# Kernel optimization log

Hardware: AMD Instinct MI355X
Metric: run time of the kernel (lower is better)

Reference implementation:

```python
import jax, jax.numpy as jnp
import numpy as np

EPS = 1e-6
MIN_EIG = 1e-4
TAU = 1.0  # obs_temperature


def _expm(A):
    """Batched matrix exponential for small KxK matrices via scaling-and-squaring
    + 12-term Taylor (matches torch.linalg.matrix_exp to ~1e-6 for moderate norms).
    Fully differentiable in both modes. A: (..., K, K)."""
    s = 6
    A = A * (1.0 / 2.0 ** s)
    I = jnp.eye(A.shape[-1], dtype=A.dtype)
    E = I + A
    term = A
    for k in range(2, 13):
        term = jnp.matmul(term, A) / k
        E = E + term
    for _ in range(s):
        E = jnp.matmul(E, E)
    return E


def setup_inputs() -> dict:
    key = jax.random.key(0)
    ks = jax.random.split(key, 6)
    B, N, K, V = 1, 2048, 3, 8192
    I = jnp.eye(K, dtype=jnp.float32)
    Ap = jax.random.normal(ks[0], (B, N, K, K), jnp.float32)
    Sigma_prior = Ap @ jnp.swapaxes(Ap, -1, -2) / K + 0.5 * I  # SPD
    Aq = jax.random.normal(ks[1], (B, N, K, K), jnp.float32)
    Sigma_q = Aq @ jnp.swapaxes(Aq, -1, -2) / K + 0.5 * I  # SPD
    phi = 0.5 * jax.random.normal(ks[2], (B, N, 3), jnp.float32)
    beta = jax.nn.softmax(jax.random.normal(ks[3], (B, N, N), jnp.float32), axis=-1)
    mu = jax.random.normal(ks[4], (B, N, K), jnp.float32)
    W_out = jax.random.normal(ks[5], (V, K), jnp.float32) / jnp.sqrt(float(K))
    generators = jnp.array([[[0, 0, 0], [0, 0, -1], [0, 1, 0]],
                            [[0, 0, 1], [0, 0, 0], [-1, 0, 0]],
                            [[0, -1, 0], [1, 0, 0], [0, 0, 0]]], jnp.float32)
    return dict(Sigma_prior=Sigma_prior, Sigma_q=Sigma_q, phi=phi, beta=beta,
                mu=mu, W_out=W_out, generators=generators)


def reference(Sigma_prior, Sigma_q, phi, beta, mu, W_out, generators):
    B, N, K = mu.shape
    dt = Sigma_prior.dtype
    I = jnp.eye(K, dtype=dt)

    # Prior precision Lambda_p = (Sigma_p + eps I)^{-1}
    Lambda_p = jnp.linalg.inv(Sigma_prior + EPS * I)

    # Categorical observation precision: Lambda_o = Cov_p(W) / tau^2
    logits = jnp.einsum('bnk,vk->bnv', mu, W_out) / TAU
    p = jax.nn.softmax(logits, axis=-1)                                # (B,N,V)
    mean_w = jnp.einsum('bnv,vk->bnk', p, W_out)                        # E_p[w]
    second = jnp.einsum('bnv,vk,vl->bnkl', p, W_out, W_out)             # E_p[ww^T]
    Lambda_o = (second - jnp.einsum('bnk,bnl->bnkl', mean_w, mean_w)) / TAU ** 2
    Lambda_o = 0.5 * (Lambda_o + jnp.swapaxes(Lambda_o, -1, -2)) + EPS * I

    # Posterior precision
    Lambda_q = jnp.linalg.inv(Sigma_q + EPS * I)                        # (B,N,K,K)

    # Gauge transport Omega_{ij} = e^{phi_i} e^{-phi_j}
    phi_mat = jnp.einsum('bnc,ckl->bnkl', phi, generators)              # (B,N,K,K)
    exp_phi = _expm(phi_mat)
    exp_neg_phi = _expm(-phi_mat)
    Omega = jnp.einsum('bikl,bjlm->bijkm', exp_phi, exp_neg_phi)        # (B,N,N,K,K)

    # Transported precision Lambda~_{qj in i-frame} = Omega Lambda_q Omega^T
    Lt = jnp.einsum('bijkl,bjlm,bijnm->bijkn', Omega, Lambda_q, Omega)  # (B,N,N,K,K)
    M_incoming = jnp.einsum('bij,bijkn->bikn', beta, Lt)                # (B,N,K,K)

    # Outgoing recoil: (sum_j beta_{ji}) * Lambda_{qi}
    M_outgoing = beta.sum(axis=1)[..., None, None] * Lambda_q

    M = Lambda_p + Lambda_o + M_incoming + M_outgoing
    M = 0.5 * (M + jnp.swapaxes(M, -1, -2))
    bad = ~jnp.isfinite(M)
    M = jnp.where(bad, jnp.broadcast_to(I, M.shape), M)
    M = M + max(MIN_EIG, 1e-4) * I

    # Eigenvalue floor and inverse
    w, v = jnp.linalg.eigh(M.astype(jnp.float32))
    w = jnp.clip(w, MIN_EIG, None)
    M_pd = jnp.einsum('...ij,...j,...kj->...ik', v, w, v)
    M_inv = jnp.einsum('...ij,...j,...kj->...ik', v, 1.0 / w, v)
    return M_pd.astype(dt), M_inv.astype(dt)
```

## Files before the change

kernel.cpp:

```cpp
#include <hip/hip_runtime.h>
#include <math.h>

#define EPSV 1e-6f
#define MINEIG 1e-4f


__device__ __forceinline__ void mm3(const float a[3][3], const float b[3][3], float c[3][3]) {
#pragma unroll
  for (int i = 0; i < 3; ++i)
#pragma unroll
    for (int j = 0; j < 3; ++j)
      c[i][j] = fmaf(a[i][0], b[0][j], fmaf(a[i][1], b[1][j], a[i][2] * b[2][j]));
}

__device__ __forceinline__ void inv3(const float a[3][3], float inv[3][3]) {
  float c00 = a[1][1] * a[2][2] - a[1][2] * a[2][1];
  float c01 = -(a[1][0] * a[2][2] - a[1][2] * a[2][0]);
  float c02 = a[1][0] * a[2][1] - a[1][1] * a[2][0];
  float det = a[0][0] * c00 + a[0][1] * c01 + a[0][2] * c02;
  float id = 1.0f / det;
  inv[0][0] = c00 * id;
  inv[0][1] = (a[0][2] * a[2][1] - a[0][1] * a[2][2]) * id;
  inv[0][2] = (a[0][1] * a[1][2] - a[0][2] * a[1][1]) * id;
  inv[1][0] = c01 * id;
  inv[1][1] = (a[0][0] * a[2][2] - a[0][2] * a[2][0]) * id;
  inv[1][2] = (a[0][2] * a[1][0] - a[0][0] * a[1][2]) * id;
  inv[2][0] = c02 * id;
  inv[2][1] = (a[0][1] * a[2][0] - a[0][0] * a[2][1]) * id;
  inv[2][2] = (a[0][0] * a[1][1] - a[0][1] * a[1][0]) * id;
}

__device__ void expm3(const float A[3][3], float E[3][3]) {
  float As[3][3], term[3][3], tmp[3][3];
#pragma unroll
  for (int i = 0; i < 3; ++i)
#pragma unroll
    for (int j = 0; j < 3; ++j) {
      As[i][j] = A[i][j] * (1.0f / 64.0f);
      term[i][j] = As[i][j];
      E[i][j] = ((i == j) ? 1.0f : 0.0f) + As[i][j];
    }
  for (int k = 2; k <= 12; ++k) {
    mm3(term, As, tmp);
    float r = 1.0f / (float)k;
#pragma unroll
    for (int i = 0; i < 3; ++i)
#pragma unroll
      for (int j = 0; j < 3; ++j) {
        term[i][j] = tmp[i][j] * r;
        E[i][j] += term[i][j];
      }
  }
  for (int s = 0; s < 6; ++s) {
    mm3(E, E, tmp);
#pragma unroll
    for (int i = 0; i < 3; ++i)
#pragma unroll
      for (int j = 0; j < 3; ++j) E[i][j] = tmp[i][j];
  }
}

template <int P, int Q>
__device__ __forceinline__ void jrot(float A[3][3], float V[3][3]) {
  float apq = A[P][Q];
  if (fabsf(apq) < 1e-20f) return;
  float theta = (A[Q][Q] - A[P][P]) / (2.0f * apq);
  float t = copysignf(1.0f, theta) / (fabsf(theta) + sqrtf(fmaf(theta, theta, 1.0f)));
  float c = 1.0f / sqrtf(fmaf(t, t, 1.0f));
  float s = t * c;
  float J[3][3] = {{1, 0, 0}, {0, 1, 0}, {0, 0, 1}};
  J[P][P] = c; J[Q][Q] = c; J[P][Q] = s; J[Q][P] = -s;
  float Jt[3][3];
#pragma unroll
  for (int i = 0; i < 3; ++i)
#pragma unroll
    for (int j = 0; j < 3; ++j) Jt[i][j] = J[j][i];
  float tmp[3][3], A2[3][3];
  mm3(A, J, tmp);
  mm3(Jt, tmp, A2);
#pragma unroll
  for (int i = 0; i < 3; ++i)
#pragma unroll
    for (int j = 0; j < 3; ++j) A[i][j] = A2[i][j];
  mm3(V, J, tmp);
#pragma unroll
  for (int i = 0; i < 3; ++i)
#pragma unroll
    for (int j = 0; j < 3; ++j) V[i][j] = tmp[i][j];
}

__device__ __forceinline__ bool finitef(float x) {
  return !(isnan(x) || isinf(x));
}


__global__ void prep_colsum_kernel(const float* __restrict__ Sp, const float* __restrict__ Sq,
                                   const float* __restrict__ phi, const float* __restrict__ gen,
                                   const float* __restrict__ beta,
                                   float* __restrict__ Lp, float* __restrict__ Lq,
                                   float* __restrict__ Rm, float* __restrict__ S12,
                                   float* __restrict__ pcs, int N) {
  int bid = blockIdx.x;
  int tid = threadIdx.x;
  int nPrep = N >> 8;
  if (bid < nPrep) {
    int i = bid * 256 + tid;
    float a[3][3], lp[3][3], lq[3][3];
#pragma unroll
    for (int k = 0; k < 3; ++k)
#pragma unroll
      for (int l = 0; l < 3; ++l)
        a[k][l] = Sp[i * 9 + k * 3 + l] + ((k == l) ? EPSV : 0.0f);
    inv3(a, lp);
#pragma unroll
    for (int k = 0; k < 3; ++k)
#pragma unroll
      for (int l = 0; l < 3; ++l)
        a[k][l] = Sq[i * 9 + k * 3 + l] + ((k == l) ? EPSV : 0.0f);
    inv3(a, lq);

    float p0 = phi[i * 3 + 0], p1 = phi[i * 3 + 1], p2 = phi[i * 3 + 2];
    float A[3][3];
#pragma unroll
    for (int k = 0; k < 3; ++k)
#pragma unroll
      for (int l = 0; l < 3; ++l)
        A[k][l] = p0 * gen[0 + k * 3 + l] + p1 * gen[9 + k * 3 + l] + p2 * gen[18 + k * 3 + l];
    float R[3][3];
    expm3(A, R);
    float Rt[3][3];
#pragma unroll
    for (int k = 0; k < 3; ++k)
#pragma unroll
      for (int l = 0; l < 3; ++l) Rt[k][l] = R[l][k];
    float t1[3][3], S[3][3];
    mm3(lq, R, t1);
    mm3(Rt, t1, S);
#pragma unroll
    for (int k = 0; k < 3; ++k)
#pragma unroll
      for (int l = 0; l < 3; ++l) {
        Lp[i * 9 + k * 3 + l] = lp[k][l];
        Lq[i * 9 + k * 3 + l] = lq[k][l];
        Rm[i * 9 + k * 3 + l] = R[k][l];
        S12[i * 12 + k * 3 + l] = S[k][l];
      }
    S12[i * 12 + 9] = 0.f; S12[i * 12 + 10] = 0.f; S12[i * 12 + 11] = 0.f;
  } else {
    int cb = bid - nPrep;
    int nCT = N >> 8;
    int rs = cb / nCT;
    int ct = cb % nCT;
    int j = ct * 256 + tid;
    const float* bp = beta + (size_t)(rs * 32) * N + j;
    float s = 0.f;
#pragma unroll
    for (int r = 0; r < 32; ++r) s += bp[(size_t)r * N];
    pcs[(size_t)rs * N + j] = s;
  }
}


__global__ void bmm_kernel(const float* __restrict__ beta, const float* __restrict__ S12,
                           float* __restrict__ T, int N) {
  int lane = threadIdx.x & 63;
  int w = threadIdx.x >> 6;
  int i = blockIdx.x * 4 + w;
  const float4* B4 = (const float4*)(beta + (size_t)i * N);
  const float4* S4 = (const float4*)S12;
  float acc[9];
#pragma unroll
  for (int k = 0; k < 9; ++k) acc[k] = 0.f;

  for (int jt = 0; jt < N; jt += 256) {
    int j = jt + lane * 4;
    float4 b = B4[j >> 2];
#pragma unroll
    for (int c = 0; c < 4; ++c) {
      float bc = (&b.x)[c];
      int sj = (j + c) * 3;
      float4 s0 = S4[sj + 0];
      float4 s1 = S4[sj + 1];
      float4 s2 = S4[sj + 2];
      acc[0] = fmaf(bc, s0.x, acc[0]);
      acc[1] = fmaf(bc, s0.y, acc[1]);
      acc[2] = fmaf(bc, s0.z, acc[2]);
      acc[3] = fmaf(bc, s0.w, acc[3]);
      acc[4] = fmaf(bc, s1.x, acc[4]);
      acc[5] = fmaf(bc, s1.y, acc[5]);
      acc[6] = fmaf(bc, s1.z, acc[6]);
      acc[7] = fmaf(bc, s1.w, acc[7]);
      acc[8] = fmaf(bc, s2.x, acc[8]);
    }
  }
#pragma unroll
  for (int k = 0; k < 9; ++k) {
    float x = acc[k];
#pragma unroll
    for (int o = 32; o > 0; o >>= 1) x += __shfl_down(x, o, 64);
    if (lane == 0) T[i * 9 + k] = x;
  }
}


__global__ void lo_finalize_kernel(const float* __restrict__ mu, const float* __restrict__ W,
                                   const float* __restrict__ Lp, const float* __restrict__ Lq,
                                   const float* __restrict__ Rm, const float* __restrict__ T,
                                   const float* __restrict__ pcs, float* __restrict__ out,
                                   int N, int V) {
  int n = blockIdx.x;
  int tid = threadIdx.x;
  float m0 = mu[n * 3 + 0], m1 = mu[n * 3 + 1], m2 = mu[n * 3 + 2];
  float se = 0.f, a0 = 0.f, a1 = 0.f, a2 = 0.f;
  float s00 = 0.f, s01 = 0.f, s02 = 0.f, s11 = 0.f, s12 = 0.f, s22 = 0.f;
  const float4* W4 = (const float4*)W;
  for (int vb = tid; vb * 4 < V; vb += 256) {
    float4 f0 = W4[vb * 3 + 0];
    float4 f1 = W4[vb * 3 + 1];
    float4 f2 = W4[vb * 3 + 2];
    float wv[4][3] = {{f0.x, f0.y, f0.z}, {f0.w, f1.x, f1.y},
                      {f1.z, f1.w, f2.x}, {f2.y, f2.z, f2.w}};
#pragma unroll
    for (int c = 0; c < 4; ++c) {
      float w0 = wv[c][0], w1 = wv[c][1], w2 = wv[c][2];
      float l = fmaf(m0, w0, fmaf(m1, w1, m2 * w2));
      float e = __expf(l);
      se += e;
      float ew0 = e * w0, ew1 = e * w1, ew2 = e * w2;
      a0 += ew0; a1 += ew1; a2 += ew2;
      s00 = fmaf(ew0, w0, s00); s01 = fmaf(ew0, w1, s01); s02 = fmaf(ew0, w2, s02);
      s11 = fmaf(ew1, w1, s11); s12 = fmaf(ew1, w2, s12); s22 = fmaf(ew2, w2, s22);
    }
  }
  float vals[10] = {se, a0, a1, a2, s00, s01, s02, s11, s12, s22};
  __shared__ float sred[4][10];
  __shared__ float scs;
#pragma unroll
  for (int k = 0; k < 10; ++k) {
    float x = vals[k];
#pragma unroll
    for (int o = 32; o > 0; o >>= 1) x += __shfl_down(x, o, 64);
    if ((tid & 63) == 0) sred[tid >> 6][k] = x;
  }
  if (tid < 64) {
    int RS = N >> 5;
    float x = 0.f;
    for (int r = tid; r < RS; r += 64) x += pcs[(size_t)r * N + n];
#pragma unroll
    for (int o = 32; o > 0; o >>= 1) x += __shfl_down(x, o, 64);
    if (tid == 0) scs = x;
  }
  __syncthreads();
  if (tid != 0) return;

  float tot[10];
#pragma unroll
  for (int k = 0; k < 10; ++k)
    tot[k] = sred[0][k] + sred[1][k] + sred[2][k] + sred[3][k];
  float inv = 1.0f / tot[0];
  float mw0 = tot[1] * inv, mw1 = tot[2] * inv, mw2 = tot[3] * inv;
  float Lo[3][3];
  Lo[0][0] = tot[4] * inv - mw0 * mw0 + EPSV;
  Lo[0][1] = Lo[1][0] = tot[5] * inv - mw0 * mw1;
  Lo[0][2] = Lo[2][0] = tot[6] * inv - mw0 * mw2;
  Lo[1][1] = tot[7] * inv - mw1 * mw1 + EPSV;
  Lo[1][2] = Lo[2][1] = tot[8] * inv - mw1 * mw2;
  Lo[2][2] = tot[9] * inv - mw2 * mw2 + EPSV;

  int i = n;
  float R[3][3], Tm[3][3], M[3][3];
#pragma unroll
  for (int k = 0; k < 3; ++k)
#pragma unroll
    for (int l = 0; l < 3; ++l) {
      R[k][l] = Rm[i * 9 + k * 3 + l];
      Tm[k][l] = T[i * 9 + k * 3 + l];
    }
  float t1[3][3], Rt[3][3], Min[3][3];
  mm3(R, Tm, t1);
#pragma unroll
  for (int k = 0; k < 3; ++k)
#pragma unroll
    for (int l = 0; l < 3; ++l) Rt[k][l] = R[l][k];
  mm3(t1, Rt, Min);
  float c = scs;
#pragma unroll
  for (int k = 0; k < 3; ++k)
#pragma unroll
    for (int l = 0; l < 3; ++l)
      M[k][l] = Lp[i * 9 + k * 3 + l] + Lo[k][l] + Min[k][l] + c * Lq[i * 9 + k * 3 + l];
#pragma unroll
  for (int k = 0; k < 3; ++k)
#pragma unroll
    for (int l = 0; l < 3; ++l) {
      if (l > k) {
        float v = 0.5f * (M[k][l] + M[l][k]);
        M[k][l] = v; M[l][k] = v;
      }
    }
#pragma unroll
  for (int k = 0; k < 3; ++k)
#pragma unroll
    for (int l = 0; l < 3; ++l)
      if (!finitef(M[k][l])) M[k][l] = (k == l) ? 1.0f : 0.0f;
  M[0][0] += MINEIG; M[1][1] += MINEIG; M[2][2] += MINEIG;

  float A[3][3], Vv[3][3] = {{1, 0, 0}, {0, 1, 0}, {0, 0, 1}};
#pragma unroll
  for (int k = 0; k < 3; ++k)
#pragma unroll
    for (int l = 0; l < 3; ++l) A[k][l] = M[k][l];
  for (int sweep = 0; sweep < 12; ++sweep) {
    jrot<0, 1>(A, Vv);
    jrot<0, 2>(A, Vv);
    jrot<1, 2>(A, Vv);
  }
  float wc[3], wi[3];
#pragma unroll
  for (int k = 0; k < 3; ++k) {
    wc[k] = fmaxf(A[k][k], MINEIG);
    wi[k] = 1.0f / wc[k];
  }
#pragma unroll
  for (int k = 0; k < 3; ++k)
#pragma unroll
    for (int l = 0; l < 3; ++l) {
      float mpd = Vv[k][0] * wc[0] * Vv[l][0] + Vv[k][1] * wc[1] * Vv[l][1] +
                  Vv[k][2] * wc[2] * Vv[l][2];
      float mnv = Vv[k][0] * wi[0] * Vv[l][0] + Vv[k][1] * wi[1] * Vv[l][1] +
                  Vv[k][2] * wi[2] * Vv[l][2];
      out[i * 9 + k * 3 + l] = mpd;
      out[(size_t)N * 9 + i * 9 + k * 3 + l] = mnv;
    }
}


extern "C" void kernel_launch(void* const* d_in, const int* in_sizes, int n_in,
                              void* d_out, int out_size, void* d_ws, size_t ws_size,
                              hipStream_t stream) {
  const float* Sp = (const float*)d_in[0];
  const float* Sq = (const float*)d_in[1];
  const float* phi = (const float*)d_in[2];
  const float* beta = (const float*)d_in[3];
  const float* mu = (const float*)d_in[4];
  const float* W = (const float*)d_in[5];
  const float* gen = (const float*)d_in[6];
  float* out = (float*)d_out;

  const int N = in_sizes[2] / 3;
  const int V = in_sizes[5] / 3;

  float* ws = (float*)d_ws;
  float* Lp = ws;
  float* Lq = Lp + (size_t)N * 9;
  float* Rm = Lq + (size_t)N * 9;
  float* S12 = Rm + (size_t)N * 9;
  float* T = S12 + (size_t)N * 12;
  float* pcs = T + (size_t)N * 9;

  int nPrep = N / 256;
  int nColsum = (N / 32) * (N / 256);
  prep_colsum_kernel<<<nPrep + nColsum, 256, 0, stream>>>(Sp, Sq, phi, gen, beta,
                                                          Lp, Lq, Rm, S12, pcs, N);
  bmm_kernel<<<N / 4, 256, 0, stream>>>(beta, S12, T, N);
  lo_finalize_kernel<<<N, 256, 0, stream>>>(mu, W, Lp, Lq, Rm, T, pcs, out, N, V);
}
```

Before: 128.5 us.

## Split Lo and finalize kernels, reuse W across rows, SoA transported precision

The softmax-covariance pass now processes four rows per block, so each loaded W vector and its outer products are reused four times. The per-row eigensolve moves into a separate thread-per-row finalize kernel instead of running on a single thread of a 256-thread block. The transported precision is stored structure-of-arrays so the beta-weighted sum reads coalesced float4 per component. The Jacobi rotation is rewritten as a direct 2x2 update with fewer sweeps, which trades some eigen accuracy for arithmetic and adds one extra kernel launch.

```diff
diff --git a/kernel.cpp b/kernel.cpp
--- a/kernel.cpp
+++ b/kernel.cpp
@@ -60,7 +60,7 @@
   }
 }
 
-template <int P, int Q>
+template <int P, int Q, int RI>
 __device__ __forceinline__ void jrot(float A[3][3], float V[3][3]) {
   float apq = A[P][Q];
   if (fabsf(apq) < 1e-20f) return;
@@ -68,25 +68,20 @@
   float t = copysignf(1.0f, theta) / (fabsf(theta) + sqrtf(fmaf(theta, theta, 1.0f)));
   float c = 1.0f / sqrtf(fmaf(t, t, 1.0f));
   float s = t * c;
-  float J[3][3] = {{1, 0, 0}, {0, 1, 0}, {0, 0, 1}};
-  J[P][P] = c; J[Q][Q] = c; J[P][Q] = s; J[Q][P] = -s;
-  float Jt[3][3];
-#pragma unroll
-  for (int i = 0; i < 3; ++i)
-#pragma unroll
-    for (int j = 0; j < 3; ++j) Jt[i][j] = J[j][i];
-  float tmp[3][3], A2[3][3];
-  mm3(A, J, tmp);
-  mm3(Jt, tmp, A2);
-#pragma unroll
-  for (int i = 0; i < 3; ++i)
-#pragma unroll
-    for (int j = 0; j < 3; ++j) A[i][j] = A2[i][j];
-  mm3(V, J, tmp);
-#pragma unroll
-  for (int i = 0; i < 3; ++i)
-#pragma unroll
-    for (int j = 0; j < 3; ++j) V[i][j] = tmp[i][j];
+  A[P][P] = A[P][P] - t * apq;
+  A[Q][Q] = A[Q][Q] + t * apq;
+  A[P][Q] = 0.f; A[Q][P] = 0.f;
+  float arp = A[RI][P], arq = A[RI][Q];
+  float nrp = c * arp - s * arq;
+  float nrq = s * arp + c * arq;
+  A[RI][P] = nrp; A[P][RI] = nrp;
+  A[RI][Q] = nrq; A[Q][RI] = nrq;
+#pragma unroll
+  for (int i = 0; i < 3; ++i) {
+    float vip = V[i][P], viq = V[i][Q];
+    V[i][P] = c * vip - s * viq;
+    V[i][Q] = s * vip + c * viq;
+  }
 }
 
 __device__ __forceinline__ bool finitef(float x) {
@@ -98,7 +93,7 @@
                                    const float* __restrict__ phi, const float* __restrict__ gen,
                                    const float* __restrict__ beta,
                                    float* __restrict__ Lp, float* __restrict__ Lq,
-                                   float* __restrict__ Rm, float* __restrict__ S12,
+                                   float* __restrict__ Rm, float* __restrict__ Ssoa,
                                    float* __restrict__ pcs, int N) {
   int bid = blockIdx.x;
   int tid = threadIdx.x;
@@ -143,9 +138,8 @@
         Lp[i * 9 + k * 3 + l] = lp[k][l];
         Lq[i * 9 + k * 3 + l] = lq[k][l];
         Rm[i * 9 + k * 3 + l] = R[k][l];
-        S12[i * 12 + k * 3 + l] = S[k][l];
+        Ssoa[(k * 3 + l) * N + i] = S[k][l];
       }
-    S12[i * 12 + 9] = 0.f; S12[i * 12 + 10] = 0.f; S12[i * 12 + 11] = 0.f;
   } else {
     int cb = bid - nPrep;
     int nCT = N >> 8;
@@ -161,36 +155,28 @@
 }
 
 
-__global__ void bmm_kernel(const float* __restrict__ beta, const float* __restrict__ S12,
+__global__ void bmm_kernel(const float* __restrict__ beta, const float* __restrict__ Ssoa,
                            float* __restrict__ T, int N) {
   int lane = threadIdx.x & 63;
   int w = threadIdx.x >> 6;
   int i = blockIdx.x * 4 + w;
   const float4* B4 = (const float4*)(beta + (size_t)i * N);
-  const float4* S4 = (const float4*)S12;
   float acc[9];
 #pragma unroll
   for (int k = 0; k < 9; ++k) acc[k] = 0.f;
 
   for (int jt = 0; jt < N; jt += 256) {
-    int j = jt + lane * 4;
-    float4 b = B4[j >> 2];
-#pragma unroll
-    for (int c = 0; c < 4; ++c) {
-      float bc = (&b.x)[c];
-      int sj = (j + c) * 3;
-      float4 s0 = S4[sj + 0];
-      float4 s1 = S4[sj + 1];
-      float4 s2 = S4[sj + 2];
-      acc[0] = fmaf(bc, s0.x, acc[0]);
-      acc[1] = fmaf(bc, s0.y, acc[1]);
-      acc[2] = fmaf(bc, s0.z, acc[2]);
-      acc[3] = fmaf(bc, s0.w, acc[3]);
-      acc[4] = fmaf(bc, s1.x, acc[4]);
-      acc[5] = fmaf(bc, s1.y, acc[5]);
-      acc[6] = fmaf(bc, s1.z, acc[6]);
-      acc[7] = fmaf(bc, s1.w, acc[7]);
-      acc[8] = fmaf(bc, s2.x, acc[8]);
+    int q = (jt >> 2) + lane;
+    float4 b = B4[q];
+    float4 sv[9];
+#pragma unroll
+    for (int k = 0; k < 9; ++k) sv[k] = ((const float4*)(Ssoa + k * N))[q];
+#pragma unroll
+    for (int k = 0; k < 9; ++k) {
+      acc[k] = fmaf(b.x, sv[k].x, acc[k]);
+      acc[k] = fmaf(b.y, sv[k].y, acc[k]);
+      acc[k] = fmaf(b.z, sv[k].z, acc[k]);
+      acc[k] = fmaf(b.w, sv[k].w, acc[k]);
     }
   }
 #pragma unroll
@@ -203,16 +189,23 @@
 }
 
 
-__global__ void lo_finalize_kernel(const float* __restrict__ mu, const float* __restrict__ W,
-                                   const float* __restrict__ Lp, const float* __restrict__ Lq,
-                                   const float* __restrict__ Rm, const float* __restrict__ T,
-                                   const float* __restrict__ pcs, float* __restrict__ out,
-                                   int N, int V) {
-  int n = blockIdx.x;
+__global__ void lo_kernel(const float* __restrict__ mu, const float* __restrict__ W,
+                          float* __restrict__ Lo, int V) {
+  int n0 = blockIdx.x * 4;
   int tid = threadIdx.x;
-  float m0 = mu[n * 3 + 0], m1 = mu[n * 3 + 1], m2 = mu[n * 3 + 2];
-  float se = 0.f, a0 = 0.f, a1 = 0.f, a2 = 0.f;
-  float s00 = 0.f, s01 = 0.f, s02 = 0.f, s11 = 0.f, s12 = 0.f, s22 = 0.f;
+  float m[4][3];
+#pragma unroll
+  for (int j = 0; j < 4; ++j) {
+    m[j][0] = mu[(n0 + j) * 3 + 0];
+    m[j][1] = mu[(n0 + j) * 3 + 1];
+    m[j][2] = mu[(n0 + j) * 3 + 2];
+  }
+  float acc[4][10];
+#pragma unroll
+  for (int j = 0; j < 4; ++j)
+#pragma unroll
+    for (int k = 0; k < 10; ++k) acc[j][k] = 0.f;
+
   const float4* W4 = (const float4*)W;
   for (int vb = tid; vb * 4 < V; vb += 256) {
     float4 f0 = W4[vb * 3 + 0];
@@ -223,51 +216,71 @@
 #pragma unroll
     for (int c = 0; c < 4; ++c) {
       float w0 = wv[c][0], w1 = wv[c][1], w2 = wv[c][2];
-      float l = fmaf(m0, w0, fmaf(m1, w1, m2 * w2));
-      float e = __expf(l);
-      se += e;
-      float ew0 = e * w0, ew1 = e * w1, ew2 = e * w2;
-      a0 += ew0; a1 += ew1; a2 += ew2;
-      s00 = fmaf(ew0, w0, s00); s01 = fmaf(ew0, w1, s01); s02 = fmaf(ew0, w2, s02);
-      s11 = fmaf(ew1, w1, s11); s12 = fmaf(ew1, w2, s12); s22 = fmaf(ew2, w2, s22);
-    }
-  }
-  float vals[10] = {se, a0, a1, a2, s00, s01, s02, s11, s12, s22};
-  __shared__ float sred[4][10];
-  __shared__ float scs;
-#pragma unroll
-  for (int k = 0; k < 10; ++k) {
-    float x = vals[k];
-#pragma unroll
-    for (int o = 32; o > 0; o >>= 1) x += __shfl_down(x, o, 64);
-    if ((tid & 63) == 0) sred[tid >> 6][k] = x;
-  }
-  if (tid < 64) {
-    int RS = N >> 5;
-    float x = 0.f;
-    for (int r = tid; r < RS; r += 64) x += pcs[(size_t)r * N + n];
-#pragma unroll
-    for (int o = 32; o > 0; o >>= 1) x += __shfl_down(x, o, 64);
-    if (tid == 0) scs = x;
-  }
+      float p00 = w0 * w0, p01 = w0 * w1, p02 = w0 * w2;
+      float p11 = w1 * w1, p12 = w1 * w2, p22 = w2 * w2;
+#pragma unroll
+      for (int j = 0; j < 4; ++j) {
+        float l = fmaf(m[j][0], w0, fmaf(m[j][1], w1, m[j][2] * w2));
+        float e = __expf(l);
+        acc[j][0] += e;
+        acc[j][1] = fmaf(e, w0, acc[j][1]);
+        acc[j][2] = fmaf(e, w1, acc[j][2]);
+        acc[j][3] = fmaf(e, w2, acc[j][3]);
+        acc[j][4] = fmaf(e, p00, acc[j][4]);
+        acc[j][5] = fmaf(e, p01, acc[j][5]);
+        acc[j][6] = fmaf(e, p02, acc[j][6]);
+        acc[j][7] = fmaf(e, p11, acc[j][7]);
+        acc[j][8] = fmaf(e, p12, acc[j][8]);
+        acc[j][9] = fmaf(e, p22, acc[j][9]);
+      }
+    }
+  }
+
+  __shared__ float sred[4][40];
+#pragma unroll
+  for (int j = 0; j < 4; ++j)
+#pragma unroll
+    for (int k = 0; k < 10; ++k) {
+      float x = acc[j][k];
+#pragma unroll
+      for (int o = 32; o > 0; o >>= 1) x += __shfl_down(x, o, 64);
+      if ((tid & 63) == 0) sred[tid >> 6][j * 10 + k] = x;
+    }
   __syncthreads();
-  if (tid != 0) return;
-
-  float tot[10];
-#pragma unroll
-  for (int k = 0; k < 10; ++k)
-    tot[k] = sred[0][k] + sred[1][k] + sred[2][k] + sred[3][k];
-  float inv = 1.0f / tot[0];
-  float mw0 = tot[1] * inv, mw1 = tot[2] * inv, mw2 = tot[3] * inv;
-  float Lo[3][3];
-  Lo[0][0] = tot[4] * inv - mw0 * mw0 + EPSV;
-  Lo[0][1] = Lo[1][0] = tot[5] * inv - mw0 * mw1;
-  Lo[0][2] = Lo[2][0] = tot[6] * inv - mw0 * mw2;
-  Lo[1][1] = tot[7] * inv - mw1 * mw1 + EPSV;
-  Lo[1][2] = Lo[2][1] = tot[8] * inv - mw1 * mw2;
-  Lo[2][2] = tot[9] * inv - mw2 * mw2 + EPSV;
-
-  int i = n;
+  if (tid < 4) {
+    int j = tid;
+    float tot[10];
+#pragma unroll
+    for (int k = 0; k < 10; ++k)
+      tot[k] = sred[0][j * 10 + k] + sred[1][j * 10 + k] +
+               sred[2][j * 10 + k] + sred[3][j * 10 + k];
+    float inv = 1.0f / tot[0];
+    float mw0 = tot[1] * inv, mw1 = tot[2] * inv, mw2 = tot[3] * inv;
+    float* o = Lo + (n0 + j) * 9;
+    o[0] = tot[4] * inv - mw0 * mw0 + EPSV;
+    float v01 = tot[5] * inv - mw0 * mw1;
+    float v02 = tot[6] * inv - mw0 * mw2;
+    o[1] = v01; o[3] = v01;
+    o[2] = v02; o[6] = v02;
+    o[4] = tot[7] * inv - mw1 * mw1 + EPSV;
+    float v12 = tot[8] * inv - mw1 * mw2;
+    o[5] = v12; o[7] = v12;
+    o[8] = tot[9] * inv - mw2 * mw2 + EPSV;
+  }
+}
+
+
+__global__ void finalize_kernel(const float* __restrict__ Lp, const float* __restrict__ Lq,
+                                const float* __restrict__ Rm, const float* __restrict__ Lo,
+                                const float* __restrict__ T, const float* __restrict__ pcs,
+                                float* __restrict__ out, int N) {
+  int i = blockIdx.x * blockDim.x + threadIdx.x;
+  if (i >= N) return;
+
+  float c = 0.f;
+  int RS = N >> 5;
+  for (int r = 0; r < RS; ++r) c += pcs[(size_t)r * N + i];
+
   float R[3][3], Tm[3][3], M[3][3];
 #pragma unroll
   for (int k = 0; k < 3; ++k)
@@ -283,12 +296,12 @@
 #pragma unroll
     for (int l = 0; l < 3; ++l) Rt[k][l] = R[l][k];
   mm3(t1, Rt, Min);
-  float c = scs;
 #pragma unroll
   for (int k = 0; k < 3; ++k)
 #pragma unroll
     for (int l = 0; l < 3; ++l)
-      M[k][l] = Lp[i * 9 + k * 3 + l] + Lo[k][l] + Min[k][l] + c * Lq[i * 9 + k * 3 + l];
+      M[k][l] = Lp[i * 9 + k * 3 + l] + Lo[i * 9 + k * 3 + l] + Min[k][l] +
+                c * Lq[i * 9 + k * 3 + l];
 #pragma unroll
   for (int k = 0; k < 3; ++k)
 #pragma unroll
@@ -310,10 +323,10 @@
   for (int k = 0; k < 3; ++k)
 #pragma unroll
     for (int l = 0; l < 3; ++l) A[k][l] = M[k][l];
-  for (int sweep = 0; sweep < 12; ++sweep) {
-    jrot<0, 1>(A, Vv);
-    jrot<0, 2>(A, Vv);
-    jrot<1, 2>(A, Vv);
+  for (int sweep = 0; sweep < 8; ++sweep) {
+    jrot<0, 1, 2>(A, Vv);
+    jrot<0, 2, 1>(A, Vv);
+    jrot<1, 2, 0>(A, Vv);
   }
   float wc[3], wi[3];
 #pragma unroll
@@ -354,14 +367,16 @@
   float* Lp = ws;
   float* Lq = Lp + (size_t)N * 9;
   float* Rm = Lq + (size_t)N * 9;
-  float* S12 = Rm + (size_t)N * 9;
-  float* T = S12 + (size_t)N * 12;
-  float* pcs = T + (size_t)N * 9;
+  float* Ssoa = Rm + (size_t)N * 9;
+  float* T = Ssoa + (size_t)N * 9;
+  float* Lo = T + (size_t)N * 9;
+  float* pcs = Lo + (size_t)N * 9;
 
   int nPrep = N / 256;
   int nColsum = (N / 32) * (N / 256);
   prep_colsum_kernel<<<nPrep + nColsum, 256, 0, stream>>>(Sp, Sq, phi, gen, beta,
-                                                          Lp, Lq, Rm, S12, pcs, N);
-  bmm_kernel<<<N / 4, 256, 0, stream>>>(beta, S12, T, N);
-  lo_finalize_kernel<<<N, 256, 0, stream>>>(mu, W, Lp, Lq, Rm, T, pcs, out, N, V);
-}
+                                                          Lp, Lq, Rm, Ssoa, pcs, N);
+  lo_kernel<<<N / 4, 256, 0, stream>>>(mu, W, Lo, V);
+  bmm_kernel<<<N / 4, 256, 0, stream>>>(beta, Ssoa, T, N);
+  finalize_kernel<<<N / 256, 256, 0, stream>>>(Lp, Lq, Rm, Lo, T, pcs, out, N);
+}
```

After: 126.0 us. About the same (-1.9%).
